# Optimization experiments

Hardware: AMD Instinct MI355X
Metric: run time of the kernel (lower is better)

Reference implementation:

```python
import jax, jax.numpy as jnp
import numpy as np

K = 4
ROUTIT = 6
EPS = 1e-12  # F.normalize default eps


def l2norm(v):
    # normalize along last axis, matching F.normalize(dim=-1)
    n = jnp.linalg.norm(v, axis=-1, keepdims=True)
    return v / jnp.maximum(n, EPS)


def setup_inputs() -> dict:
    key = jax.random.key(0)
    k1, k2, k3, k4 = jax.random.split(key, 4)
    n, in_dim = 100000, 128
    m = 1600000
    d = K * 32  # k * x_dim = 128
    x = jax.random.normal(k1, (n, in_dim), dtype=jnp.float32)
    src_trg = jax.random.randint(k2, (2, m), 0, n, dtype=jnp.int64)
    # Linear(in_dim, k*x_dim) params
    lim = 1.0 / np.sqrt(in_dim)
    W = jax.random.uniform(k3, (d, in_dim), minval=-lim, maxval=lim, dtype=jnp.float32)
    b = jax.random.uniform(k4, (d,), minval=-lim, maxval=lim, dtype=jnp.float32)
    return {"x": x, "src_trg": src_trg, "W": W, "b": b}


def reference(x, src_trg, W, b):
    n = x.shape[0]
    d = W.shape[0]
    dd = d // K  # delta_d
    src, trg = src_trg[0], src_trg[1]

    h = x @ W.T + b                      # [n, d]
    h = l2norm(h.reshape(n, K, dd))      # [n, k, dd], per-channel unit norm

    z = h[src]                           # [m, k, dd] gathered source features
    c = h
    for _ in range(ROUTIT):
        # per-channel dot between source feature and current target state
        p = jnp.sum(z * c[trg], axis=2)          # [m, k]
        p = jax.nn.softmax(p, axis=1)            # route over channels
        ws = p[:, :, None] * z                   # [m, k, dd]
        c = c.at[trg].add(ws)                    # scatter-add into targets
        c = l2norm(c)                            # renormalize per channel
    return c.reshape(n, d)
```

## Files before the change

### kernel.cpp

```cpp
#include <hip/hip_runtime.h>
#include <hip/hip_fp16.h>
#include <math.h>

#define ROUTIT 6
#define CAPQ 10
#define WPB 2
#define SCB 256

typedef _Float16 half8 __attribute__((ext_vector_type(8)));
typedef float    f32x4 __attribute__((ext_vector_type(4)));

__device__ __forceinline__ int load_idx(const void* p, long long i, int is64)
{
    if (is64) return (int)((const long long*)p)[i];
    return ((const int*)p)[i];
}

template <int CTRL>
__device__ __forceinline__ float dpp_add(float x)
{
    int y = __builtin_amdgcn_update_dpp(0, __float_as_int(x), CTRL, 0xf, 0xf, true);
    return x + __int_as_float(y);
}

__device__ __forceinline__ float grpsum4(float p)
{
    p = dpp_add<0xB1>(p);
    p = dpp_add<0x4E>(p);
    return p;
}

__device__ __forceinline__ float rowtotal16(float x)
{
    x = dpp_add<0x124>(x);
    x = dpp_add<0x128>(x);
    return x;
}

__device__ __forceinline__ float rowsum16(float p)
{
    p = dpp_add<0xB1>(p);
    p = dpp_add<0x4E>(p);
    p = dpp_add<0x124>(p);
    p = dpp_add<0x128>(p);
    return p;
}

__device__ __forceinline__ float sum_x16(float x)
{
#if __has_builtin(__builtin_amdgcn_permlane16_swap)
    unsigned u = __float_as_uint(x);
    auto r = __builtin_amdgcn_permlane16_swap(u, u, false, false);
    return __uint_as_float(r[0]) + __uint_as_float(r[1]);
#else
    return x + __shfl_xor(x, 16);
#endif
}

__device__ __forceinline__ float sum_x32(float x)
{
#if __has_builtin(__builtin_amdgcn_permlane32_swap)
    unsigned u = __float_as_uint(x);
    auto r = __builtin_amdgcn_permlane32_swap(u, u, false, false);
    return __uint_as_float(r[0]) + __uint_as_float(r[1]);
#else
    return x + __shfl_xor(x, 32);
#endif
}

__device__ __forceinline__ void unpack8(uint4 q, float4& L, float4& H)
{
    __half2 h;
    h = *(__half2*)&q.x; L.x = __low2float(h); H.x = __high2float(h);
    h = *(__half2*)&q.y; L.y = __low2float(h); H.y = __high2float(h);
    h = *(__half2*)&q.z; L.z = __low2float(h); H.z = __high2float(h);
    h = *(__half2*)&q.w; L.w = __low2float(h); H.w = __high2float(h);
}

__device__ __forceinline__ void quad_acc(const float4& zL, const float4& zH,
                                         const float4& cL, const float4& cH,
                                         float4& aL, float4& aH)
{
    float p = zL.x*cL.x + zL.y*cL.y + zL.z*cL.z + zL.w*cL.w
            + zH.x*cH.x + zH.y*cH.y + zH.z*cH.z + zH.w*cH.w;
    p = grpsum4(p);
    float ex = __expf(p);
    float d  = rowtotal16(ex);
    float w  = ex * __builtin_amdgcn_rcpf(d);
    aL.x += w * zL.x;  aL.y += w * zL.y;  aL.z += w * zL.z;  aL.w += w * zL.w;
    aH.x += w * zH.x;  aH.y += w * zH.y;  aH.z += w * zH.z;  aH.w += w * zH.w;
}

__global__ __launch_bounds__(256)
void gemm_norm_mfma_kernel(const float* __restrict__ x, const float* __restrict__ W,
                           const float* __restrict__ b, unsigned* __restrict__ hh, int n)
{
    __shared__ _Float16 wlds[128 * 136];

    const int tid  = threadIdx.x;
    const int wv   = tid >> 6;
    const int lane = tid & 63;
    const int lo   = lane & 15;
    const int hi   = lane >> 4;

    for (int t = 0; t < 16; ++t) {
        int idx = (t * 256 + tid) * 4;
        int j = idx >> 7, k = idx & 127;
        float4 w4 = *(const float4*)(W + idx);
        _Float16* dst = &wlds[j * 136 + k];
        dst[0] = (_Float16)w4.x; dst[1] = (_Float16)w4.y;
        dst[2] = (_Float16)w4.z; dst[3] = (_Float16)w4.w;
    }
    __syncthreads();

    const int rowbase = blockIdx.x * 64 + wv * 16;
    int row  = rowbase + lo;
    int rowc = row < n ? row : n - 1;

    half8 afrag[4];
    #pragma unroll
    for (int q = 0; q < 4; ++q) {
        const float* src = x + (size_t)rowc * 128 + q * 32 + hi * 8;
        float4 u0 = *(const float4*)src;
        float4 u1 = *(const float4*)(src + 4);
        afrag[q][0] = (_Float16)u0.x; afrag[q][1] = (_Float16)u0.y;
        afrag[q][2] = (_Float16)u0.z; afrag[q][3] = (_Float16)u0.w;
        afrag[q][4] = (_Float16)u1.x; afrag[q][5] = (_Float16)u1.y;
        afrag[q][6] = (_Float16)u1.z; afrag[q][7] = (_Float16)u1.w;
    }

    f32x4 acc[8];
    #pragma unroll
    for (int t = 0; t < 8; ++t) {
        float bb = b[t * 16 + lo];
        acc[t][0] = bb; acc[t][1] = bb; acc[t][2] = bb; acc[t][3] = bb;
    }

    #pragma unroll
    for (int q = 0; q < 4; ++q) {
        #pragma unroll
        for (int t = 0; t < 8; ++t) {
            half8 bfrag = *(const half8*)&wlds[(t * 16 + lo) * 136 + q * 32 + hi * 8];
            acc[t] = __builtin_amdgcn_mfma_f32_16x16x32_f16(afrag[q], bfrag, acc[t], 0, 0, 0);
        }
    }

    #pragma unroll
    for (int c = 0; c < 4; ++c) {
        #pragma unroll
        for (int j = 0; j < 4; ++j) {
            float v0 = acc[2 * c][j];
            float v1 = acc[2 * c + 1][j];
            float ss = rowsum16(v0 * v0 + v1 * v1);
            float inv = __builtin_amdgcn_rcpf(fmaxf(sqrtf(ss), 1e-12f));
            int r = rowbase + hi * 4 + j;
            if (r < n) {
                __half2 pk = __floats2half2_rn(v0 * inv, v1 * inv);
                hh[(size_t)r * 64 + c * 16 + lo] = *(unsigned*)&pk;
            }
        }
    }
}

__global__ void prep_kernel(int* __restrict__ cnt, int n,
                            unsigned* __restrict__ hh,
                            int* __restrict__ edge_src, long long padcap,
                            const int* __restrict__ raw, int* __restrict__ flag)
{
    long long i = (long long)blockIdx.x * blockDim.x + threadIdx.x;
    long long stride = (long long)gridDim.x * blockDim.x;
    for (long long k = i; k < padcap; k += stride) {
        if (k < n) cnt[k] = 0;
        if (k < 64) hh[(size_t)n * 64 + k] = 0u;
        __builtin_nontemporal_store(n, &edge_src[k]);
    }
    if (i == 0) {
        int all_zero = 1;
        for (int k = 1; k < 64; k += 2)
            if (raw[k] != 0) { all_zero = 0; break; }
        *flag = all_zero;
    }
}

__global__ void hist_kernel(const void* __restrict__ st, long long m, int n,
                            const int* __restrict__ idx64, int* __restrict__ cnt)
{
    long long e4 = ((long long)blockIdx.x * blockDim.x + threadIdx.x) * 4;
    if (e4 >= m) return;
    int is64 = *idx64;
    int cnt4 = (int)((m - e4) < 4 ? (m - e4) : 4);
    int t[4];
    if (is64) {
        const long long* p = (const long long*)st + m + e4;
        if (cnt4 == 4) {
            longlong2 a = *(const longlong2*)p;
            longlong2 c = *(const longlong2*)(p + 2);
            t[0] = (int)a.x; t[1] = (int)a.y; t[2] = (int)c.x; t[3] = (int)c.y;
        } else {
            for (int i = 0; i < cnt4; ++i) t[i] = (int)p[i];
        }
    } else {
        const int* p = (const int*)st + m + e4;
        if (cnt4 == 4) {
            int4 a = *(const int4*)p;
            t[0] = a.x; t[1] = a.y; t[2] = a.z; t[3] = a.w;
        } else {
            for (int i = 0; i < cnt4; ++i) t[i] = p[i];
        }
    }
    for (int i = 0; i < cnt4; ++i)
        if (t[i] >= 0 && t[i] < n) atomicAdd(&cnt[t[i]], 1);
}

__global__ __launch_bounds__(256)
void scan_partial_kernel(const int* __restrict__ cnt, int n, int chunk,
                         int* __restrict__ bsum)
{
    int b = blockIdx.x, t = threadIdx.x;
    int lo = b * chunk, hi = min(lo + chunk, n);
    int s = 0;
    for (int i = lo + t; i < hi; i += 256) s += (cnt[i] + 3) & ~3;
    __shared__ int red[256];
    red[t] = s; __syncthreads();
    for (int off = 128; off > 0; off >>= 1) {
        if (t < off) red[t] += red[t + off];
        __syncthreads();
    }
    if (t == 0) bsum[b] = red[0];
}

__global__ __launch_bounds__(256)
void scan_offsets_kernel(const int* __restrict__ bsum, int nb,
                         int* __restrict__ boff, int* __restrict__ total)
{
    __shared__ int lds[256];
    int t = threadIdx.x;
    int v = (t < nb) ? bsum[t] : 0;
    lds[t] = v; __syncthreads();
    for (int off = 1; off < 256; off <<= 1) {
        int u = (t >= off) ? lds[t - off] : 0;
        __syncthreads();
        lds[t] += u;
        __syncthreads();
    }
    if (t < nb) boff[t] = lds[t] - v;
    if (t == 255) *total = lds[255];
}

__global__ __launch_bounds__(256)
void scan_write_kernel(const int* __restrict__ cnt, int n, int chunk,
                       const int* __restrict__ boff, const int* __restrict__ total,
                       int* __restrict__ row_ptr, int* __restrict__ cursor)
{
    int b = blockIdx.x, t = threadIdx.x;
    int lo = b * chunk, hi = min(lo + chunk, n);
    __shared__ int lds[256];
    int run = boff[b];
    for (int base = lo; base < hi; base += 256) {
        int i = base + t;
        int v = (i < hi) ? ((cnt[i] + 3) & ~3) : 0;
        lds[t] = v; __syncthreads();
        for (int off = 1; off < 256; off <<= 1) {
            int u = (t >= off) ? lds[t - off] : 0;
            __syncthreads();
            lds[t] += u;
            __syncthreads();
        }
        if (i < hi) {
            int excl = run + lds[t] - v;
            row_ptr[i] = excl;
            cursor[i]  = excl;
        }
        run += lds[255];
        __syncthreads();
    }
    if (b == 0 && t == 0) row_ptr[n] = *total;
}

__global__ void scatter_kernel(const void* __restrict__ st, long long m, int n,
                               const int* __restrict__ idx64,
                               int* __restrict__ cursor, int* __restrict__ edge_src)
{
    long long e4 = ((long long)blockIdx.x * blockDim.x + threadIdx.x) * 4;
    if (e4 >= m) return;
    int is64 = *idx64;
    int cnt4 = (int)((m - e4) < 4 ? (m - e4) : 4);
    int t[4], s[4];
    if (is64) {
        const long long* pt = (const long long*)st + m + e4;
        const long long* ps = (const long long*)st + e4;
        for (int i = 0; i < cnt4; ++i) { t[i] = (int)pt[i]; s[i] = (int)ps[i]; }
    } else {
        const int* pt = (const int*)st + m + e4;
        const int* ps = (const int*)st + e4;
        if (cnt4 == 4) {
            int4 a = *(const int4*)pt;
            int4 c = *(const int4*)ps;
            t[0] = a.x; t[1] = a.y; t[2] = a.z; t[3] = a.w;
            s[0] = c.x; s[1] = c.y; s[2] = c.z; s[3] = c.w;
        } else {
            for (int i = 0; i < cnt4; ++i) { t[i] = pt[i]; s[i] = ps[i]; }
        }
    }
    for (int i = 0; i < cnt4; ++i) {
        if (t[i] >= 0 && t[i] < n) {
            int pos = atomicAdd(&cursor[t[i]], 1);
            __builtin_nontemporal_store(s[i], &edge_src[pos]);
        }
    }
}

__global__ __launch_bounds__(64 * WPB)
void route_kernel(const unsigned* __restrict__ hh, const int* __restrict__ row_ptr,
                  const int* __restrict__ edge_src, float* __restrict__ out, int n)
{
    __shared__ uint4 zls[WPB][CAPQ][64];

    int wv   = threadIdx.x >> 6;
    int wid  = __builtin_amdgcn_readfirstlane(blockIdx.x * WPB + wv);
    int lane = threadIdx.x & 63;
    int row  = lane >> 4;
    int rl   = lane & 15;
    if (wid >= n) return;

    const uint4* __restrict__ hh4 = (const uint4*)hh;
    float4 cL, cH;
    unpack8(hh4[(size_t)wid * 16 + rl], cL, cH);

    const int e0  = row_ptr[wid];
    const int np  = (row_ptr[wid + 1] - e0) >> 2;
    const int ncp = np < CAPQ ? np : CAPQ;
    const float selfm = (row == 0) ? 1.0f : 0.0f;

    float4 aL, aH;

    aL.x = cL.x*selfm; aL.y = cL.y*selfm; aL.z = cL.z*selfm; aL.w = cL.w*selfm;
    aH.x = cH.x*selfm; aH.y = cH.y*selfm; aH.z = cH.z*selfm; aH.w = cH.w*selfm;
    for (int j = 0; j < np; ++j) {
        int s = edge_src[e0 + 4 * j + row];
        uint4 zq = hh4[(size_t)s * 16 + rl];
        if (j < ncp) zls[wv][j][lane] = zq;
        float4 zL, zH; unpack8(zq, zL, zH);
        quad_acc(zL, zH, cL, cH, aL, aH);
    }
    {
        aL.x = sum_x32(sum_x16(aL.x)); aL.y = sum_x32(sum_x16(aL.y));
        aL.z = sum_x32(sum_x16(aL.z)); aL.w = sum_x32(sum_x16(aL.w));
        aH.x = sum_x32(sum_x16(aH.x)); aH.y = sum_x32(sum_x16(aH.y));
        aH.z = sum_x32(sum_x16(aH.z)); aH.w = sum_x32(sum_x16(aH.w));
        float ss = aL.x*aL.x + aL.y*aL.y + aL.z*aL.z + aL.w*aL.w
                 + aH.x*aH.x + aH.y*aH.y + aH.z*aH.z + aH.w*aH.w;
        ss = grpsum4(ss);
        float inv = __builtin_amdgcn_rcpf(fmaxf(sqrtf(ss), 1e-12f));
        cL.x = aL.x*inv; cL.y = aL.y*inv; cL.z = aL.z*inv; cL.w = aL.w*inv;
        cH.x = aH.x*inv; cH.y = aH.y*inv; cH.z = aH.z*inv; cH.w = aH.w*inv;
    }

    #pragma unroll 1
    for (int it = 1; it < ROUTIT; ++it) {
        aL.x = cL.x*selfm; aL.y = cL.y*selfm; aL.z = cL.z*selfm; aL.w = cL.w*selfm;
        aH.x = cH.x*selfm; aH.y = cH.y*selfm; aH.z = cH.z*selfm; aH.w = cH.w*selfm;
        #pragma unroll 2
        for (int j = 0; j < ncp; ++j) {
            uint4 zq = zls[wv][j][lane];
            float4 zL, zH; unpack8(zq, zL, zH);
            quad_acc(zL, zH, cL, cH, aL, aH);
        }
        for (int j = ncp; j < np; ++j) {
            int s = edge_src[e0 + 4 * j + row];
            uint4 zq = hh4[(size_t)s * 16 + rl];
            float4 zL, zH; unpack8(zq, zL, zH);
            quad_acc(zL, zH, cL, cH, aL, aH);
        }
        aL.x = sum_x32(sum_x16(aL.x)); aL.y = sum_x32(sum_x16(aL.y));
        aL.z = sum_x32(sum_x16(aL.z)); aL.w = sum_x32(sum_x16(aL.w));
        aH.x = sum_x32(sum_x16(aH.x)); aH.y = sum_x32(sum_x16(aH.y));
        aH.z = sum_x32(sum_x16(aH.z)); aH.w = sum_x32(sum_x16(aH.w));
        float ss = aL.x*aL.x + aL.y*aL.y + aL.z*aL.z + aL.w*aL.w
                 + aH.x*aH.x + aH.y*aH.y + aH.z*aH.z + aH.w*aH.w;
        ss = grpsum4(ss);
        float inv = __builtin_amdgcn_rcpf(fmaxf(sqrtf(ss), 1e-12f));
        cL.x = aL.x*inv; cL.y = aL.y*inv; cL.z = aL.z*inv; cL.w = aL.w*inv;
        cH.x = aH.x*inv; cH.y = aH.y*inv; cH.z = aH.z*inv; cH.w = aH.w*inv;
    }

    if (row == 0) {
        int ch = rl >> 2, qo = (rl & 3) * 4;
        float* orow = out + (size_t)wid * 128 + ch * 32 + qo;
        *(float4*)orow        = cL;
        *(float4*)(orow + 16) = cH;
    }
}

extern "C" void kernel_launch(void* const* d_in, const int* in_sizes, int n_in,
                              void* d_out, int out_size, void* d_ws, size_t ws_size,
                              hipStream_t stream)
{
    const float* x       = (const float*)d_in[0];
    const void*  src_trg = d_in[1];
    const float* W       = (const float*)d_in[2];
    const float* b       = (const float*)d_in[3];
    float*       out     = (float*)d_out;

    int n = in_sizes[0] / 128;
    long long m = in_sizes[1] / 2;
    int chunk = (n + SCB - 1) / SCB;
    long long padcap = m + 3LL * n + 4;
    long long m4 = (m + 3) / 4;

    unsigned* hh    = (unsigned*)d_ws;
    int* cnt        = (int*)(hh + (size_t)(n + 1) * 64);
    int* row_ptr    = cnt + n;
    int* cursor     = row_ptr + (n + 1);
    int* edge_src   = cursor + n;
    int* idx64      = edge_src + padcap;
    int* bsum       = idx64 + 1;
    int* boff       = bsum + SCB;
    int* total      = boff + SCB;

    hipLaunchKernelGGL(gemm_norm_mfma_kernel, dim3((n + 63) / 64), dim3(256), 0, stream,
                       x, W, b, hh, n);
    hipLaunchKernelGGL(prep_kernel, dim3(2048), dim3(256), 0, stream,
                       cnt, n, hh, edge_src, padcap, (const int*)src_trg, idx64);
    hipLaunchKernelGGL(hist_kernel, dim3((int)((m4 + 255) / 256)), dim3(256), 0, stream,
                       src_trg, m, n, idx64, cnt);
    hipLaunchKernelGGL(scan_partial_kernel, dim3(SCB), dim3(256), 0, stream,
                       cnt, n, chunk, bsum);
    hipLaunchKernelGGL(scan_offsets_kernel, dim3(1), dim3(256), 0, stream,
                       bsum, SCB, boff, total);
    hipLaunchKernelGGL(scan_write_kernel, dim3(SCB), dim3(256), 0, stream,
                       cnt, n, chunk, boff, total, row_ptr, cursor);
    hipLaunchKernelGGL(scatter_kernel, dim3((int)((m4 + 255) / 256)), dim3(256), 0, stream,
                       src_trg, m, n, idx64, cursor, edge_src);
    hipLaunchKernelGGL(route_kernel, dim3((n + WPB - 1) / WPB), dim3(64 * WPB), 0, stream,
                       hh, row_ptr, edge_src, out, n);
}
```

Baseline: 506.3 us.

## Replicate histogram and cursor counters; cache unpacked fp32 edges in LDS

The histogram and scatter stages now spread their atomics over eight replicated counter arrays, chosen by thread index, to reduce contention on the same target counters. The scan sums the replicas and writes per-replica cursor bases so each target's edges stay contiguous. The route kernel now caches unpacked fp32 features in LDS instead of packed fp16, which removes the repeated unpack in later iterations. In exchange the LDS cache holds half as many edge quads per wave (5 instead of 10), and the scan stages read eight times as many counters.

```diff
diff --git a/kernel.cpp b/kernel.cpp
--- a/kernel.cpp
+++ b/kernel.cpp
@@ -3,9 +3,10 @@
 #include <math.h>
 
 #define ROUTIT 6
-#define CAPQ 10
+#define CAPQ 5
 #define WPB 2
 #define SCB 256
+#define NREP 8
 
 typedef _Float16 half8 __attribute__((ext_vector_type(8)));
 typedef float    f32x4 __attribute__((ext_vector_type(4)));
@@ -162,15 +163,16 @@
     }
 }
 
-__global__ void prep_kernel(int* __restrict__ cnt, int n,
+__global__ void prep_kernel(int* __restrict__ cntR, int n,
                             unsigned* __restrict__ hh,
                             int* __restrict__ edge_src, long long padcap,
                             const int* __restrict__ raw, int* __restrict__ flag)
 {
     long long i = (long long)blockIdx.x * blockDim.x + threadIdx.x;
     long long stride = (long long)gridDim.x * blockDim.x;
+    long long nrep = (long long)NREP * n;
     for (long long k = i; k < padcap; k += stride) {
-        if (k < n) cnt[k] = 0;
+        if (k < nrep) cntR[k] = 0;
         if (k < 64) hh[(size_t)n * 64 + k] = 0u;
         __builtin_nontemporal_store(n, &edge_src[k]);
     }
@@ -183,10 +185,13 @@
 }
 
 __global__ void hist_kernel(const void* __restrict__ st, long long m, int n,
-                            const int* __restrict__ idx64, int* __restrict__ cnt)
-{
-    long long e4 = ((long long)blockIdx.x * blockDim.x + threadIdx.x) * 4;
+                            const int* __restrict__ idx64, int* __restrict__ cntR)
+{
+    long long tidg = (long long)blockIdx.x * blockDim.x + threadIdx.x;
+    long long e4 = tidg * 4;
     if (e4 >= m) return;
+    int rep = (int)(tidg & (NREP - 1));
+    int* cnt = cntR + (size_t)rep * n;
     int is64 = *idx64;
     int cnt4 = (int)((m - e4) < 4 ? (m - e4) : 4);
     int t[4];
@@ -213,13 +218,18 @@
 }
 
 __global__ __launch_bounds__(256)
-void scan_partial_kernel(const int* __restrict__ cnt, int n, int chunk,
+void scan_partial_kernel(const int* __restrict__ cntR, int n, int chunk,
                          int* __restrict__ bsum)
 {
     int b = blockIdx.x, t = threadIdx.x;
     int lo = b * chunk, hi = min(lo + chunk, n);
     int s = 0;
-    for (int i = lo + t; i < hi; i += 256) s += (cnt[i] + 3) & ~3;
+    for (int i = lo + t; i < hi; i += 256) {
+        int tot = 0;
+        #pragma unroll
+        for (int r = 0; r < NREP; ++r) tot += cntR[(size_t)r * n + i];
+        s += (tot + 3) & ~3;
+    }
     __shared__ int red[256];
     red[t] = s; __syncthreads();
     for (int off = 128; off > 0; off >>= 1) {
@@ -248,9 +258,9 @@
 }
 
 __global__ __launch_bounds__(256)
-void scan_write_kernel(const int* __restrict__ cnt, int n, int chunk,
+void scan_write_kernel(const int* __restrict__ cntR, int n, int chunk,
                        const int* __restrict__ boff, const int* __restrict__ total,
-                       int* __restrict__ row_ptr, int* __restrict__ cursor)
+                       int* __restrict__ row_ptr, int* __restrict__ cursorR)
 {
     int b = blockIdx.x, t = threadIdx.x;
     int lo = b * chunk, hi = min(lo + chunk, n);
@@ -258,7 +268,15 @@
     int run = boff[b];
     for (int base = lo; base < hi; base += 256) {
         int i = base + t;
-        int v = (i < hi) ? ((cnt[i] + 3) & ~3) : 0;
+        int c[NREP], tot = 0;
+        if (i < hi) {
+            #pragma unroll
+            for (int r = 0; r < NREP; ++r) {
+                c[r] = cntR[(size_t)r * n + i];
+                tot += c[r];
+            }
+        }
+        int v = (i < hi) ? ((tot + 3) & ~3) : 0;
         lds[t] = v; __syncthreads();
         for (int off = 1; off < 256; off <<= 1) {
             int u = (t >= off) ? lds[t - off] : 0;
@@ -269,7 +287,12 @@
         if (i < hi) {
             int excl = run + lds[t] - v;
             row_ptr[i] = excl;
-            cursor[i]  = excl;
+            int pos = excl;
+            #pragma unroll
+            for (int r = 0; r < NREP; ++r) {
+                cursorR[(size_t)r * n + i] = pos;
+                pos += c[r];
+            }
         }
         run += lds[255];
         __syncthreads();
@@ -279,10 +302,13 @@
 
 __global__ void scatter_kernel(const void* __restrict__ st, long long m, int n,
                                const int* __restrict__ idx64,
-                               int* __restrict__ cursor, int* __restrict__ edge_src)
-{
-    long long e4 = ((long long)blockIdx.x * blockDim.x + threadIdx.x) * 4;
+                               int* __restrict__ cursorR, int* __restrict__ edge_src)
+{
+    long long tidg = (long long)blockIdx.x * blockDim.x + threadIdx.x;
+    long long e4 = tidg * 4;
     if (e4 >= m) return;
+    int rep = (int)(tidg & (NREP - 1));
+    int* cursor = cursorR + (size_t)rep * n;
     int is64 = *idx64;
     int cnt4 = (int)((m - e4) < 4 ? (m - e4) : 4);
     int t[4], s[4];
@@ -314,7 +340,8 @@
 void route_kernel(const unsigned* __restrict__ hh, const int* __restrict__ row_ptr,
                   const int* __restrict__ edge_src, float* __restrict__ out, int n)
 {
-    __shared__ uint4 zls[WPB][CAPQ][64];
+    __shared__ float4 zlsA[WPB][CAPQ][64];
+    __shared__ float4 zlsB[WPB][CAPQ][64];
 
     int wv   = threadIdx.x >> 6;
     int wid  = __builtin_amdgcn_readfirstlane(blockIdx.x * WPB + wv);
@@ -339,8 +366,11 @@
     for (int j = 0; j < np; ++j) {
         int s = edge_src[e0 + 4 * j + row];
         uint4 zq = hh4[(size_t)s * 16 + rl];
-        if (j < ncp) zls[wv][j][lane] = zq;
         float4 zL, zH; unpack8(zq, zL, zH);
+        if (j < ncp) {
+            zlsA[wv][j][lane] = zL;
+            zlsB[wv][j][lane] = zH;
+        }
         quad_acc(zL, zH, cL, cH, aL, aH);
     }
     {
@@ -362,8 +392,8 @@
         aH.x = cH.x*selfm; aH.y = cH.y*selfm; aH.z = cH.z*selfm; aH.w = cH.w*selfm;
         #pragma unroll 2
         for (int j = 0; j < ncp; ++j) {
-            uint4 zq = zls[wv][j][lane];
-            float4 zL, zH; unpack8(zq, zL, zH);
+            float4 zL = zlsA[wv][j][lane];
+            float4 zH = zlsB[wv][j][lane];
             quad_acc(zL, zH, cL, cH, aL, aH);
         }
         for (int j = ncp; j < np; ++j) {
@@ -409,10 +439,10 @@
     long long m4 = (m + 3) / 4;
 
     unsigned* hh    = (unsigned*)d_ws;
-    int* cnt        = (int*)(hh + (size_t)(n + 1) * 64);
-    int* row_ptr    = cnt + n;
-    int* cursor     = row_ptr + (n + 1);
-    int* edge_src   = cursor + n;
+    int* cntR       = (int*)(hh + (size_t)(n + 1) * 64);
+    int* row_ptr    = cntR + (size_t)NREP * n;
+    int* cursorR    = row_ptr + (n + 1);
+    int* edge_src   = cursorR + (size_t)NREP * n;
     int* idx64      = edge_src + padcap;
     int* bsum       = idx64 + 1;
     int* boff       = bsum + SCB;
@@ -421,17 +451,17 @@
     hipLaunchKernelGGL(gemm_norm_mfma_kernel, dim3((n + 63) / 64), dim3(256), 0, stream,
                        x, W, b, hh, n);
     hipLaunchKernelGGL(prep_kernel, dim3(2048), dim3(256), 0, stream,
-                       cnt, n, hh, edge_src, padcap, (const int*)src_trg, idx64);
+                       cntR, n, hh, edge_src, padcap, (const int*)src_trg, idx64);
     hipLaunchKernelGGL(hist_kernel, dim3((int)((m4 + 255) / 256)), dim3(256), 0, stream,
-                       src_trg, m, n, idx64, cnt);
+                       src_trg, m, n, idx64, cntR);
     hipLaunchKernelGGL(scan_partial_kernel, dim3(SCB), dim3(256), 0, stream,
-                       cnt, n, chunk, bsum);
+                       cntR, n, chunk, bsum);
     hipLaunchKernelGGL(scan_offsets_kernel, dim3(1), dim3(256), 0, stream,
                        bsum, SCB, boff, total);
     hipLaunchKernelGGL(scan_write_kernel, dim3(SCB), dim3(256), 0, stream,
-                       cnt, n, chunk, boff, total, row_ptr, cursor);
+                       cntR, n, chunk, boff, total, row_ptr, cursorR);
     hipLaunchKernelGGL(scatter_kernel, dim3((int)((m4 + 255) / 256)), dim3(256), 0, stream,
-                       src_trg, m, n, idx64, cursor, edge_src);
+                       src_trg, m, n, idx64, cursorR, edge_src);
     hipLaunchKernelGGL(route_kernel, dim3((n + WPB - 1) / WPB), dim3(64 * WPB), 0, stream,
                        hh, row_ptr, edge_src, out, n);
 }
```

Measured after the change: 498.0 us. Within noise of the previous version (-1.6%).
